# Kernel optimization log

Measured on AMD Instinct MI355X. Metric: run time of the kernel, lower is better.

The kernel has to match this reference:

```python
import jax, jax.numpy as jnp
import numpy as np
import math

B, L, D = 2, 2048, 1024
H = 16
DH = D // H  # 64
XPOS_SCALE_BASE = 512.0
THETA = 10000.0


def setup_inputs() -> dict:
    key = jax.random.key(0)
    ks = jax.random.split(key, 9)
    s = 0.02  # keep logits in a sane range like trained weights
    return {
        "x": jax.random.normal(ks[0], (B, L, D), dtype=jnp.float32),
        "Wq": jax.random.normal(ks[1], (D, D), dtype=jnp.float32) * s,
        "bq": jax.random.normal(ks[2], (D,), dtype=jnp.float32) * s,
        "Wk": jax.random.normal(ks[3], (D, D), dtype=jnp.float32) * s,
        "bk": jax.random.normal(ks[4], (D,), dtype=jnp.float32) * s,
        "Wv": jax.random.normal(ks[5], (D, D), dtype=jnp.float32) * s,
        "bv": jax.random.normal(ks[6], (D,), dtype=jnp.float32) * s,
        "Wo": jax.random.normal(ks[7], (D, D), dtype=jnp.float32) * s,
        "bo": jax.random.normal(ks[8], (D,), dtype=jnp.float32) * s,
    }


def _rotate_half(t):
    # pairwise interleaved rotation, as in rotary_embedding_torch
    t1 = t[..., 0::2]
    t2 = t[..., 1::2]
    return jnp.stack([-t2, t1], axis=-1).reshape(t.shape)


def _xpos_rotate(q, k):
    # q, k: [B, H, L, DH]; xPos rotary embedding (use_xpos=True)
    seq = q.shape[2]
    half = jnp.arange(0, DH, 2, dtype=jnp.float32)
    inv_freq = 1.0 / (THETA ** (half / DH))            # [DH/2]
    t = jnp.arange(seq, dtype=jnp.float32)             # [L]
    freqs = t[:, None] * inv_freq[None, :]             # [L, DH/2]
    freqs = jnp.repeat(freqs, 2, axis=-1)              # [L, DH] interleaved
    # xPos length-extrapolatable scale
    scale_vec = (half + 0.4 * DH) / (1.4 * DH)         # [DH/2]
    power = (t - seq // 2) / XPOS_SCALE_BASE           # [L]
    scale = scale_vec[None, :] ** power[:, None]       # [L, DH/2]
    scale = jnp.repeat(scale, 2, axis=-1)              # [L, DH]
    cos = jnp.cos(freqs)
    sin = jnp.sin(freqs)
    q_out = q * (cos * scale) + _rotate_half(q) * (sin * scale)
    k_out = k * (cos / scale) + _rotate_half(k) * (sin / scale)
    return q_out, k_out


def reference(x, Wq, bq, Wk, bk, Wv, bv, Wo, bo):
    b, l, d = x.shape
    # projections; note source swaps names: v_mat <- k-proj, k_mat <- v-proj
    q = (x @ Wq.T + bq).reshape(b, l, H, DH).transpose(0, 2, 1, 3)  # [b,h,l,dh]
    v = (x @ Wk.T + bk).reshape(b, l, H, DH).transpose(0, 2, 1, 3)
    k = (x @ Wv.T + bv).reshape(b, l, H, DH).transpose(0, 2, 1, 3)
    q, k = _xpos_rotate(q, k)
    # source divides by sqrt(Dh * num_heads) == sqrt(dim)
    scores = jnp.einsum("bhqd,bhkd->bhqk", q, k) / math.sqrt(d)
    weights = jax.nn.softmax(scores, axis=-1)
    inter = jnp.einsum("bhqk,bhkd->bhqd", weights, v)
    inter = inter.transpose(0, 2, 1, 3).reshape(b, l, d)
    return inter @ Wo.T + bo
```

## Files before the change

### kernel.cpp

```cpp
#include <hip/hip_runtime.h>
#include <math.h>

#define NB 2
#define NL 2048
#define ND 1024
#define NH 16
#define NDH 64
#define NBL 4096

typedef __attribute__((ext_vector_type(4)))  float f32x4;
typedef __attribute__((ext_vector_type(16))) float f32x16;
typedef __attribute__((ext_vector_type(8)))  short s16x8;
typedef __attribute__((ext_vector_type(4)))  short s16x4;

#define LOG2E 1.44269504088896f

__device__ __forceinline__ float fexp2(float x){
#if __has_builtin(__builtin_amdgcn_exp2f)
  return __builtin_amdgcn_exp2f(x);
#else
  return exp2f(x);
#endif
}

__device__ __forceinline__ unsigned short f2bf(float f){
  unsigned int u = __float_as_uint(f);
  u += 0x7FFF + ((u >> 16) & 1);
  return (unsigned short)(u >> 16);
}

__device__ __forceinline__ unsigned int pk2bf(float lo, float hi){
  return __builtin_amdgcn_perm(__float_as_uint(hi) + 0x8000u,
                               __float_as_uint(lo) + 0x8000u, 0x07060302u);
}

__global__ void cvt_all(const float* __restrict__ x,
                        const float* __restrict__ wq, const float* __restrict__ wk,
                        const float* __restrict__ wv, const float* __restrict__ wo,
                        unsigned short* __restrict__ xb,
                        unsigned short* __restrict__ wqb, unsigned short* __restrict__ wkb,
                        unsigned short* __restrict__ wvb, unsigned short* __restrict__ wob){
  int i = blockIdx.x * blockDim.x + threadIdx.x;
  const float* s; unsigned short* d; int off;
  if (i < (1<<20)) { s = x; d = xb; off = i; }
  else {
    int j = i - (1<<20); int w = j >> 18; off = j & ((1<<18)-1);
    s = (w==0)?wq:(w==1)?wk:(w==2)?wv:wo;
    d = (w==0)?wqb:(w==1)?wkb:(w==2)?wvb:wob;
  }
  float4 f = reinterpret_cast<const float4*>(s)[off];
  ushort4 r; r.x=f2bf(f.x); r.y=f2bf(f.y); r.z=f2bf(f.z); r.w=f2bf(f.w);
  reinterpret_cast<ushort4*>(d)[off] = r;
}

__global__ void rope_tables(float2* __restrict__ qtab, float2* __restrict__ ktab){
  int t = blockIdx.x * blockDim.x + threadIdx.x;
  int l = t >> 5, i = t & 31;
  float half = 2.0f * (float)i;
  float inv_freq = 1.0f / powf(10000.0f, half / 64.0f);
  float fr = (float)l * inv_freq;
  float sv = (half + 0.4f * 64.0f) / (1.4f * 64.0f);
  float pw = ((float)l - 1024.0f) / 512.0f;
  float sc = powf(sv, pw);
  float cs = cosf(fr), sn = sinf(fr);
  qtab[t] = make_float2(cs * sc, sn * sc);
  ktab[t] = make_float2(cs / sc, sn / sc);
}

__device__ __forceinline__ void gemm_core128(
    const unsigned short* __restrict__ A, const unsigned short* __restrict__ W,
    int row0, int col0,
    unsigned short (&As)[128][32], unsigned short (&Bs)[128][32],
    f32x4 (&acc)[4][4])
{
  const int tid  = threadIdx.x;
  const int wave = tid >> 6, lane = tid & 63;
  const int m16  = lane & 15, quad = lane >> 4;
  const int mrow = (wave & 1) * 64, ncol = (wave >> 1) * 64;
  const int rA   = lane >> 2, cA = (lane & 3) * 8;

  for (int k0 = 0; k0 < ND; k0 += 32){
    __syncthreads();
#pragma unroll
    for (int i2 = 0; i2 < 2; i2++){
      const int c = wave * 2 + i2;
      const unsigned short* ga = A + (size_t)(row0 + c*16 + rA) * ND + k0 + cA;
      const unsigned short* gb = W + (size_t)(col0 + c*16 + rA) * ND + k0 + cA;
      __builtin_amdgcn_global_load_lds((const __attribute__((address_space(1))) void*)ga,
                                       (__attribute__((address_space(3))) void*)&As[c*16][0], 16, 0, 0);
      __builtin_amdgcn_global_load_lds((const __attribute__((address_space(1))) void*)gb,
                                       (__attribute__((address_space(3))) void*)&Bs[c*16][0], 16, 0, 0);
    }
    __syncthreads();
    s16x8 af[4], bf[4];
#pragma unroll
    for (int mt = 0; mt < 4; mt++) af[mt] = *reinterpret_cast<const s16x8*>(&As[mrow + mt*16 + m16][quad*8]);
#pragma unroll
    for (int nt = 0; nt < 4; nt++) bf[nt] = *reinterpret_cast<const s16x8*>(&Bs[ncol + nt*16 + m16][quad*8]);
#pragma unroll
    for (int mt = 0; mt < 4; mt++)
#pragma unroll
      for (int nt = 0; nt < 4; nt++)
        acc[mt][nt] = __builtin_amdgcn_mfma_f32_16x16x32_bf16(af[mt], bf[nt], acc[mt][nt], 0, 0, 0);
  }
}

__global__ __launch_bounds__(256) void gemm_qkv(
    const unsigned short* __restrict__ A,
    const unsigned short* __restrict__ Wq, const float* __restrict__ bq,
    const unsigned short* __restrict__ Wk, const float* __restrict__ bk,
    const unsigned short* __restrict__ Wv, const float* __restrict__ bv,
    unsigned short* __restrict__ qb, unsigned short* __restrict__ kb,
    unsigned short* __restrict__ vtb,
    const float2* __restrict__ qtab, const float2* __restrict__ ktab)
{
  __shared__ unsigned short As[128][32];
  __shared__ unsigned short Bs[128][32];
  __shared__ unsigned short T[128][72];

  const int mode = blockIdx.z;
  const unsigned short* W = (mode==0) ? Wq : (mode==1) ? Wk : Wv;
  const float* bias       = (mode==0) ? bq : (mode==1) ? bk : bv;

  const int row0 = blockIdx.x * 128, col0 = blockIdx.y * 128;
  f32x4 acc[4][4] = {};
  gemm_core128(A, W, row0, col0, As, Bs, acc);

  const int tid  = threadIdx.x;
  const int wave = tid >> 6, lane = tid & 63;
  const int m16  = lane & 15, quad = lane >> 4;
  const int mrow = (wave & 1) * 64, ncol = (wave >> 1) * 64;

  if (mode == 2){
    const int b = row0 >> 11, l0 = row0 & (NL - 1);
#pragma unroll
    for (int h2 = 0; h2 < 2; h2++){
      __syncthreads();
      if ((wave >> 1) == h2){
#pragma unroll
        for (int mt = 0; mt < 4; mt++)
#pragma unroll
          for (int nt = 0; nt < 4; nt++)
#pragma unroll
            for (int r = 0; r < 4; r++){
              int lrow = mrow + mt*16 + quad*4 + r;
              int dh   = nt*16 + m16;
              T[lrow][dh] = f2bf(acc[mt][nt][r] + bias[col0 + h2*64 + dh]);
            }
      }
      __syncthreads();
      const int bh = b * NH + (col0 >> 6) + h2;
#pragma unroll
      for (int j4 = 0; j4 < 4; j4++){
        int c = tid * 4 + j4;
        int d = c >> 4, seg = (c & 15) * 8;
        unsigned short tmp[8];
#pragma unroll
        for (int jj = 0; jj < 8; jj++) tmp[jj] = T[seg + jj][d];
        *reinterpret_cast<uint4*>(vtb + (size_t)(bh * NDH + d) * NL + l0 + seg) =
            *reinterpret_cast<uint4*>(tmp);
      }
    }
  } else {
    const float qscale = (mode == 0) ? (0.03125f * LOG2E) : 1.0f;
    const float2* tab  = (mode == 0) ? qtab : ktab;
    unsigned short* dst = (mode == 0) ? qb : kb;
#pragma unroll
    for (int mt = 0; mt < 4; mt++)
#pragma unroll
      for (int nt = 0; nt < 4; nt++)
#pragma unroll
        for (int r = 0; r < 4; r++){
          int grow = row0 + mrow + mt*16 + quad*4 + r;
          int gcol = col0 + ncol + nt*16 + m16;
          float v = acc[mt][nt][r] + bias[gcol];
          int b = grow >> 11, l = grow & (NL - 1);
          int h = gcol >> 6, dh = gcol & 63;
          float pv = __shfl_xor(v, 1);
          float2 t = tab[l*32 + (dh >> 1)];
          float rh = (dh & 1) ? pv : -pv;
          float ov = (v * t.x + rh * t.y) * qscale;
          dst[(((size_t)(b * NH + h)) * NL + l) * NDH + dh] = f2bf(ov);
        }
  }
}

__global__ __launch_bounds__(256) void gemm_o(
    const unsigned short* __restrict__ A, const unsigned short* __restrict__ W,
    const float* __restrict__ bias, float* __restrict__ out)
{
  __shared__ unsigned short As[128][32];
  __shared__ unsigned short Bs[64][32];
  const int tid  = threadIdx.x;
  const int wave = tid >> 6, lane = tid & 63;
  const int m16  = lane & 15, quad = lane >> 4;
  const int mrow = (wave & 1) * 64, ncol = (wave >> 1) * 32;
  const int rA   = lane >> 2, cA = (lane & 3) * 8;
  const int row0 = blockIdx.x * 128, col0 = blockIdx.y * 64;

  f32x4 acc[4][2] = {};

  for (int k0 = 0; k0 < ND; k0 += 32){
    __syncthreads();
#pragma unroll
    for (int i3 = 0; i3 < 3; i3++){
      const int c = wave * 3 + i3;
      const unsigned short* g; unsigned short* l;
      if (c < 8){ g = A + (size_t)(row0 + c*16 + rA) * ND + k0 + cA;      l = &As[c*16][0]; }
      else      { g = W + (size_t)(col0 + (c-8)*16 + rA) * ND + k0 + cA;  l = &Bs[(c-8)*16][0]; }
      __builtin_amdgcn_global_load_lds((const __attribute__((address_space(1))) void*)g,
                                       (__attribute__((address_space(3))) void*)l, 16, 0, 0);
    }
    __syncthreads();
    s16x8 af[4], bf[2];
#pragma unroll
    for (int mt = 0; mt < 4; mt++) af[mt] = *reinterpret_cast<const s16x8*>(&As[mrow + mt*16 + m16][quad*8]);
#pragma unroll
    for (int nt = 0; nt < 2; nt++) bf[nt] = *reinterpret_cast<const s16x8*>(&Bs[ncol + nt*16 + m16][quad*8]);
#pragma unroll
    for (int mt = 0; mt < 4; mt++)
#pragma unroll
      for (int nt = 0; nt < 2; nt++)
        acc[mt][nt] = __builtin_amdgcn_mfma_f32_16x16x32_bf16(af[mt], bf[nt], acc[mt][nt], 0, 0, 0);
  }

#pragma unroll
  for (int mt = 0; mt < 4; mt++)
#pragma unroll
    for (int nt = 0; nt < 2; nt++)
#pragma unroll
      for (int r = 0; r < 4; r++){
        int grow = row0 + mrow + mt*16 + quad*4 + r;
        int gcol = col0 + ncol + nt*16 + m16;
        out[(size_t)grow * ND + gcol] = acc[mt][nt][r] + bias[gcol];
      }
}

__global__ __launch_bounds__(256, 1) void attn_kernel(
    const unsigned short* __restrict__ qb,
    const unsigned short* __restrict__ kb,
    const unsigned short* __restrict__ vtb,
    unsigned short* __restrict__ ob)
{
  __shared__ unsigned short smem[256 * 72];
  const int tid  = threadIdx.x;
  const int wave = tid >> 6, lane = tid & 63;
  const int l31  = lane & 31, g = lane >> 5;
  const int bh   = blockIdx.y;
  const int q0   = blockIdx.x * 256;
  const unsigned short* Q  = qb  + (size_t)bh * NL * NDH;
  const unsigned short* K  = kb  + (size_t)bh * NL * NDH;
  const unsigned short* Vt = vtb + (size_t)bh * NDH * NL;

  s16x8 qf[2][4];
#pragma unroll
  for (int q2 = 0; q2 < 2; q2++)
#pragma unroll
    for (int s = 0; s < 4; s++)
      qf[q2][s] = *reinterpret_cast<const s16x8*>(
          Q + (size_t)(q0 + wave*64 + q2*32 + l31) * NDH + s*16 + g*8);

  const int r0 = tid >> 3,          c0 = tid & 7;
  const int r1 = (tid + 256) >> 3,  c1 = tid & 7;
  const int so0 = r0*64 + ((c0 ^ (r0 & 7)) * 8);
  const int so1 = r1*64 + ((c1 ^ (r1 & 7)) * 8);

  uint4 kreg0 = *reinterpret_cast<const uint4*>(K  + (size_t)r0 * NDH + c0*8);
  uint4 kreg1 = *reinterpret_cast<const uint4*>(K  + (size_t)r1 * NDH + c1*8);
  uint4 vreg0 = *reinterpret_cast<const uint4*>(Vt + (size_t)r0 * NL  + c0*8);
  uint4 vreg1 = *reinterpret_cast<const uint4*>(Vt + (size_t)r1 * NL  + c1*8);
  *reinterpret_cast<uint4*>(&smem[so0])         = kreg0;
  *reinterpret_cast<uint4*>(&smem[so1])         = kreg1;
  *reinterpret_cast<uint4*>(&smem[8192 + so0])  = vreg0;
  *reinterpret_cast<uint4*>(&smem[8192 + so1])  = vreg1;
  kreg0 = *reinterpret_cast<const uint4*>(K  + (size_t)(64 + r0) * NDH + c0*8);
  kreg1 = *reinterpret_cast<const uint4*>(K  + (size_t)(64 + r1) * NDH + c1*8);
  vreg0 = *reinterpret_cast<const uint4*>(Vt + (size_t)r0 * NL + 64 + c0*8);
  vreg1 = *reinterpret_cast<const uint4*>(Vt + (size_t)r1 * NL + 64 + c1*8);
  __syncthreads();

  float ls[2] = {0.f, 0.f};
  f32x16 ot[2][2] = {};
  const int key7 = l31 & 7;

  for (int kt = 0; kt < 32; kt++){
    const int cur = (kt & 1) * 4096;
    const int nxt = 4096 - cur;
    if (kt < 31){
      *reinterpret_cast<uint4*>(&smem[nxt + so0])        = kreg0;
      *reinterpret_cast<uint4*>(&smem[nxt + so1])        = kreg1;
      *reinterpret_cast<uint4*>(&smem[8192 + nxt + so0]) = vreg0;
      *reinterpret_cast<uint4*>(&smem[8192 + nxt + so1]) = vreg1;
    }
    if (kt < 30){
      const int k0n = (kt + 2) * 64;
      kreg0 = *reinterpret_cast<const uint4*>(K  + (size_t)(k0n + r0) * NDH + c0*8);
      kreg1 = *reinterpret_cast<const uint4*>(K  + (size_t)(k0n + r1) * NDH + c1*8);
      vreg0 = *reinterpret_cast<const uint4*>(Vt + (size_t)r0 * NL + k0n + c0*8);
      vreg1 = *reinterpret_cast<const uint4*>(Vt + (size_t)r1 * NL + k0n + c1*8);
    }

    const unsigned short* Kb = &smem[cur];
    const unsigned short* Vb = &smem[8192 + cur];

    unsigned int pe[2][2][8];
#pragma unroll
    for (int t = 0; t < 2; t++){
      f32x16 st0 = {}, st1 = {};
#pragma unroll
      for (int s = 0; s < 4; s++){
        const int cg = (2*s + g) ^ key7;
        s16x8 kf = *reinterpret_cast<const s16x8*>(&Kb[(t*32 + l31)*64 + cg*8]);
        st0 = __builtin_amdgcn_mfma_f32_32x32x16_bf16(kf, qf[0][s], st0, 0, 0, 0);
        st1 = __builtin_amdgcn_mfma_f32_32x32x16_bf16(kf, qf[1][s], st1, 0, 0, 0);
      }
#pragma unroll
      for (int i = 0; i < 8; i++){
        float a0 = fexp2(st0[2*i]), a1 = fexp2(st0[2*i+1]);
        ls[0] += a0 + a1;
        pe[0][t][i] = pk2bf(a0, a1);
        float b0 = fexp2(st1[2*i]), b1 = fexp2(st1[2*i+1]);
        ls[1] += b0 + b1;
        pe[1][t][i] = pk2bf(b0, b1);
      }
    }

#pragma unroll
    for (int mt = 0; mt < 2; mt++){
      const int dh = mt*32 + l31;
#pragma unroll
      for (int s = 0; s < 8; s++){
        const int cg = s ^ (dh & 7);
        s16x4 vf = *reinterpret_cast<const s16x4*>(&Vb[dh*64 + cg*8 + g*4]);
        uint2 pb0; pb0.x = pe[0][s>>2][2*(s&3)]; pb0.y = pe[0][s>>2][2*(s&3)+1];
        ot[mt][0] = __builtin_amdgcn_mfma_f32_32x32x8bf16_1k(
            vf, *reinterpret_cast<s16x4*>(&pb0), ot[mt][0], 0, 0, 0);
        uint2 pb1; pb1.x = pe[1][s>>2][2*(s&3)]; pb1.y = pe[1][s>>2][2*(s&3)+1];
        ot[mt][1] = __builtin_amdgcn_mfma_f32_32x32x8bf16_1k(
            vf, *reinterpret_cast<s16x4*>(&pb1), ot[mt][1], 0, 0, 0);
      }
    }
    __syncthreads();
  }

  float linv[2];
#pragma unroll
  for (int q2 = 0; q2 < 2; q2++){
    float t = ls[q2] + __shfl_xor(ls[q2], 32);
    linv[q2] = 1.0f / t;
  }

#pragma unroll
  for (int mt = 0; mt < 2; mt++)
#pragma unroll
    for (int q2 = 0; q2 < 2; q2++)
#pragma unroll
      for (int s = 0; s < 4; s++){
        float o0 = ot[mt][q2][4*s    ] * linv[q2];
        float o1 = ot[mt][q2][4*s + 1] * linv[q2];
        float o2 = ot[mt][q2][4*s + 2] * linv[q2];
        float o3 = ot[mt][q2][4*s + 3] * linv[q2];
        uint2 pk; pk.x = pk2bf(o0, o1); pk.y = pk2bf(o2, o3);
        *reinterpret_cast<uint2*>(&smem[(wave*64 + q2*32 + l31)*72 + mt*32 + s*8 + g*4]) = pk;
      }
  __syncthreads();

  const int bb = bh >> 4, h = bh & 15;
#pragma unroll
  for (int j = 0; j < 8; j++){
    int idx = j*256 + tid;
    int row = idx >> 3, cg2 = (idx & 7) * 8;
    *reinterpret_cast<uint4*>(ob + ((size_t)(bb*NL + q0 + row)) * ND + h*NDH + cg2) =
        *reinterpret_cast<const uint4*>(&smem[row*72 + cg2]);
  }
}

extern "C" void kernel_launch(void* const* d_in, const int* in_sizes, int n_in,
                              void* d_out, int out_size, void* d_ws, size_t ws_size,
                              hipStream_t stream)
{
  (void)in_sizes; (void)n_in; (void)out_size; (void)ws_size;
  const float* x  = (const float*)d_in[0];
  const float* Wq = (const float*)d_in[1];
  const float* bq = (const float*)d_in[2];
  const float* Wk = (const float*)d_in[3];
  const float* bk = (const float*)d_in[4];
  const float* Wv = (const float*)d_in[5];
  const float* bv = (const float*)d_in[6];
  const float* Wo = (const float*)d_in[7];
  const float* bo = (const float*)d_in[8];
  float* out = (float*)d_out;

  char* p = (char*)d_ws;
  unsigned short* xb   = (unsigned short*)p; p += (size_t)NBL*ND*2;
  unsigned short* wqb  = (unsigned short*)p; p += (size_t)ND*ND*2;
  unsigned short* wkb  = (unsigned short*)p; p += (size_t)ND*ND*2;
  unsigned short* wvb  = (unsigned short*)p; p += (size_t)ND*ND*2;
  unsigned short* wob  = (unsigned short*)p; p += (size_t)ND*ND*2;
  unsigned short* qbuf = (unsigned short*)p; p += (size_t)NBL*ND*2;
  unsigned short* kbuf = (unsigned short*)p; p += (size_t)NBL*ND*2;
  unsigned short* vtb  = (unsigned short*)p; p += (size_t)NBL*ND*2;
  unsigned short* ibuf = (unsigned short*)p; p += (size_t)NBL*ND*2;
  float2* qtab = (float2*)p; p += (size_t)NL*32*8;
  float2* ktab = (float2*)p; p += (size_t)NL*32*8;

  hipLaunchKernelGGL(cvt_all, dim3(8192), dim3(256), 0, stream,
                     x, Wq, Wk, Wv, Wo, xb, wqb, wkb, wvb, wob);
  hipLaunchKernelGGL(rope_tables, dim3(NL*32/256), dim3(256), 0, stream, qtab, ktab);

  hipLaunchKernelGGL(gemm_qkv, dim3(NBL/128, ND/128, 3), dim3(256), 0, stream,
                     xb, wqb, bq, wvb, bv, wkb, bk, qbuf, kbuf, vtb, qtab, ktab);

  hipLaunchKernelGGL(attn_kernel, dim3(NL/256, NB*NH), dim3(256), 0, stream,
                     qbuf, kbuf, vtb, ibuf);

  hipLaunchKernelGGL(gemm_o, dim3(NBL/128, ND/64), dim3(256), 0, stream, ibuf, wob, bo, out);
}
```

Before: 208.9 us.

## Split attention over key halves and add a combine kernel

Splits each attention block's key range into two halves via a third grid dimension, doubling the number of blocks, and allows two blocks per CU. Each half writes unnormalized bf16 partial outputs and row sums; a new combine kernel adds the partials and normalizes before the output projection. This targets the low occupancy of one block per CU in the attention kernel. In exchange it adds an extra kernel pass over the partial buffers and an extra bf16 rounding of partials. The P-fragment packing is also reorganized into uint2 pairs.

```diff
diff --git a/kernel.cpp b/kernel.cpp
--- a/kernel.cpp
+++ b/kernel.cpp
@@ -236,18 +236,21 @@
       }
 }
 
-__global__ __launch_bounds__(256, 1) void attn_kernel(
+__global__ __launch_bounds__(256, 2) void attn_kernel(
     const unsigned short* __restrict__ qb,
     const unsigned short* __restrict__ kb,
     const unsigned short* __restrict__ vtb,
-    unsigned short* __restrict__ ob)
+    unsigned short* __restrict__ opart,
+    float* __restrict__ lsum)
 {
   __shared__ unsigned short smem[256 * 72];
   const int tid  = threadIdx.x;
   const int wave = tid >> 6, lane = tid & 63;
   const int l31  = lane & 31, g = lane >> 5;
   const int bh   = blockIdx.y;
+  const int z    = blockIdx.z;
   const int q0   = blockIdx.x * 256;
+  const int kbase = z * (NL / 2);
   const unsigned short* Q  = qb  + (size_t)bh * NL * NDH;
   const unsigned short* K  = kb  + (size_t)bh * NL * NDH;
   const unsigned short* Vt = vtb + (size_t)bh * NDH * NL;
@@ -260,50 +263,50 @@
       qf[q2][s] = *reinterpret_cast<const s16x8*>(
           Q + (size_t)(q0 + wave*64 + q2*32 + l31) * NDH + s*16 + g*8);
 
-  const int r0 = tid >> 3,          c0 = tid & 7;
-  const int r1 = (tid + 256) >> 3,  c1 = tid & 7;
+  const int r0 = tid >> 3, c0 = tid & 7;
+  const int r1 = r0 + 32;
   const int so0 = r0*64 + ((c0 ^ (r0 & 7)) * 8);
-  const int so1 = r1*64 + ((c1 ^ (r1 & 7)) * 8);
-
-  uint4 kreg0 = *reinterpret_cast<const uint4*>(K  + (size_t)r0 * NDH + c0*8);
-  uint4 kreg1 = *reinterpret_cast<const uint4*>(K  + (size_t)r1 * NDH + c1*8);
-  uint4 vreg0 = *reinterpret_cast<const uint4*>(Vt + (size_t)r0 * NL  + c0*8);
-  uint4 vreg1 = *reinterpret_cast<const uint4*>(Vt + (size_t)r1 * NL  + c1*8);
+  const int so1 = r1*64 + ((c0 ^ (r1 & 7)) * 8);
+
+  uint4 kreg0 = *reinterpret_cast<const uint4*>(K  + (size_t)(kbase + r0) * NDH + c0*8);
+  uint4 kreg1 = *reinterpret_cast<const uint4*>(K  + (size_t)(kbase + r1) * NDH + c0*8);
+  uint4 vreg0 = *reinterpret_cast<const uint4*>(Vt + (size_t)r0 * NL + kbase + c0*8);
+  uint4 vreg1 = *reinterpret_cast<const uint4*>(Vt + (size_t)r1 * NL + kbase + c0*8);
   *reinterpret_cast<uint4*>(&smem[so0])         = kreg0;
   *reinterpret_cast<uint4*>(&smem[so1])         = kreg1;
   *reinterpret_cast<uint4*>(&smem[8192 + so0])  = vreg0;
   *reinterpret_cast<uint4*>(&smem[8192 + so1])  = vreg1;
-  kreg0 = *reinterpret_cast<const uint4*>(K  + (size_t)(64 + r0) * NDH + c0*8);
-  kreg1 = *reinterpret_cast<const uint4*>(K  + (size_t)(64 + r1) * NDH + c1*8);
-  vreg0 = *reinterpret_cast<const uint4*>(Vt + (size_t)r0 * NL + 64 + c0*8);
-  vreg1 = *reinterpret_cast<const uint4*>(Vt + (size_t)r1 * NL + 64 + c1*8);
+  kreg0 = *reinterpret_cast<const uint4*>(K  + (size_t)(kbase + 64 + r0) * NDH + c0*8);
+  kreg1 = *reinterpret_cast<const uint4*>(K  + (size_t)(kbase + 64 + r1) * NDH + c0*8);
+  vreg0 = *reinterpret_cast<const uint4*>(Vt + (size_t)r0 * NL + kbase + 64 + c0*8);
+  vreg1 = *reinterpret_cast<const uint4*>(Vt + (size_t)r1 * NL + kbase + 64 + c0*8);
   __syncthreads();
 
   float ls[2] = {0.f, 0.f};
   f32x16 ot[2][2] = {};
   const int key7 = l31 & 7;
 
-  for (int kt = 0; kt < 32; kt++){
+  for (int kt = 0; kt < 16; kt++){
     const int cur = (kt & 1) * 4096;
     const int nxt = 4096 - cur;
-    if (kt < 31){
+    if (kt < 15){
       *reinterpret_cast<uint4*>(&smem[nxt + so0])        = kreg0;
       *reinterpret_cast<uint4*>(&smem[nxt + so1])        = kreg1;
       *reinterpret_cast<uint4*>(&smem[8192 + nxt + so0]) = vreg0;
       *reinterpret_cast<uint4*>(&smem[8192 + nxt + so1]) = vreg1;
     }
-    if (kt < 30){
-      const int k0n = (kt + 2) * 64;
+    if (kt < 14){
+      const int k0n = kbase + (kt + 2) * 64;
       kreg0 = *reinterpret_cast<const uint4*>(K  + (size_t)(k0n + r0) * NDH + c0*8);
-      kreg1 = *reinterpret_cast<const uint4*>(K  + (size_t)(k0n + r1) * NDH + c1*8);
+      kreg1 = *reinterpret_cast<const uint4*>(K  + (size_t)(k0n + r1) * NDH + c0*8);
       vreg0 = *reinterpret_cast<const uint4*>(Vt + (size_t)r0 * NL + k0n + c0*8);
-      vreg1 = *reinterpret_cast<const uint4*>(Vt + (size_t)r1 * NL + k0n + c1*8);
+      vreg1 = *reinterpret_cast<const uint4*>(Vt + (size_t)r1 * NL + k0n + c0*8);
     }
 
     const unsigned short* Kb = &smem[cur];
     const unsigned short* Vb = &smem[8192 + cur];
 
-    unsigned int pe[2][2][8];
+    uint2 pmat[2][8];
 #pragma unroll
     for (int t = 0; t < 2; t++){
       f32x16 st0 = {}, st1 = {};
@@ -315,13 +318,17 @@
         st1 = __builtin_amdgcn_mfma_f32_32x32x16_bf16(kf, qf[1][s], st1, 0, 0, 0);
       }
 #pragma unroll
-      for (int i = 0; i < 8; i++){
-        float a0 = fexp2(st0[2*i]), a1 = fexp2(st0[2*i+1]);
-        ls[0] += a0 + a1;
-        pe[0][t][i] = pk2bf(a0, a1);
-        float b0 = fexp2(st1[2*i]), b1 = fexp2(st1[2*i+1]);
-        ls[1] += b0 + b1;
-        pe[1][t][i] = pk2bf(b0, b1);
+      for (int j = 0; j < 4; j++){
+        float a0 = fexp2(st0[4*j]), a1 = fexp2(st0[4*j+1]);
+        float a2 = fexp2(st0[4*j+2]), a3 = fexp2(st0[4*j+3]);
+        ls[0] += (a0 + a1) + (a2 + a3);
+        pmat[0][t*4+j].x = pk2bf(a0, a1);
+        pmat[0][t*4+j].y = pk2bf(a2, a3);
+        float b0 = fexp2(st1[4*j]), b1 = fexp2(st1[4*j+1]);
+        float b2 = fexp2(st1[4*j+2]), b3 = fexp2(st1[4*j+3]);
+        ls[1] += (b0 + b1) + (b2 + b3);
+        pmat[1][t*4+j].x = pk2bf(b0, b1);
+        pmat[1][t*4+j].y = pk2bf(b2, b3);
       }
     }
 
@@ -332,22 +339,20 @@
       for (int s = 0; s < 8; s++){
         const int cg = s ^ (dh & 7);
         s16x4 vf = *reinterpret_cast<const s16x4*>(&Vb[dh*64 + cg*8 + g*4]);
-        uint2 pb0; pb0.x = pe[0][s>>2][2*(s&3)]; pb0.y = pe[0][s>>2][2*(s&3)+1];
         ot[mt][0] = __builtin_amdgcn_mfma_f32_32x32x8bf16_1k(
-            vf, *reinterpret_cast<s16x4*>(&pb0), ot[mt][0], 0, 0, 0);
-        uint2 pb1; pb1.x = pe[1][s>>2][2*(s&3)]; pb1.y = pe[1][s>>2][2*(s&3)+1];
+            vf, *reinterpret_cast<s16x4*>(&pmat[0][s]), ot[mt][0], 0, 0, 0);
         ot[mt][1] = __builtin_amdgcn_mfma_f32_32x32x8bf16_1k(
-            vf, *reinterpret_cast<s16x4*>(&pb1), ot[mt][1], 0, 0, 0);
+            vf, *reinterpret_cast<s16x4*>(&pmat[1][s]), ot[mt][1], 0, 0, 0);
       }
     }
     __syncthreads();
   }
 
-  float linv[2];
 #pragma unroll
   for (int q2 = 0; q2 < 2; q2++){
     float t = ls[q2] + __shfl_xor(ls[q2], 32);
-    linv[q2] = 1.0f / t;
+    if (g == 0)
+      lsum[((size_t)z * NB * NH + bh) * NL + q0 + wave*64 + q2*32 + l31] = t;
   }
 
 #pragma unroll
@@ -356,23 +361,50 @@
     for (int q2 = 0; q2 < 2; q2++)
 #pragma unroll
       for (int s = 0; s < 4; s++){
-        float o0 = ot[mt][q2][4*s    ] * linv[q2];
-        float o1 = ot[mt][q2][4*s + 1] * linv[q2];
-        float o2 = ot[mt][q2][4*s + 2] * linv[q2];
-        float o3 = ot[mt][q2][4*s + 3] * linv[q2];
-        uint2 pk; pk.x = pk2bf(o0, o1); pk.y = pk2bf(o2, o3);
+        uint2 pk;
+        pk.x = pk2bf(ot[mt][q2][4*s], ot[mt][q2][4*s + 1]);
+        pk.y = pk2bf(ot[mt][q2][4*s + 2], ot[mt][q2][4*s + 3]);
         *reinterpret_cast<uint2*>(&smem[(wave*64 + q2*32 + l31)*72 + mt*32 + s*8 + g*4]) = pk;
       }
   __syncthreads();
 
   const int bb = bh >> 4, h = bh & 15;
+  unsigned short* od = opart + (size_t)z * NBL * ND;
 #pragma unroll
   for (int j = 0; j < 8; j++){
     int idx = j*256 + tid;
     int row = idx >> 3, cg2 = (idx & 7) * 8;
-    *reinterpret_cast<uint4*>(ob + ((size_t)(bb*NL + q0 + row)) * ND + h*NDH + cg2) =
+    *reinterpret_cast<uint4*>(od + ((size_t)(bb*NL + q0 + row)) * ND + h*NDH + cg2) =
         *reinterpret_cast<const uint4*>(&smem[row*72 + cg2]);
   }
+}
+
+__device__ __forceinline__ unsigned int comb2(unsigned int a, unsigned int b, float inv){
+  float alo = __uint_as_float(a << 16), ahi = __uint_as_float(a & 0xFFFF0000u);
+  float blo = __uint_as_float(b << 16), bhi = __uint_as_float(b & 0xFFFF0000u);
+  return pk2bf((alo + blo) * inv, (ahi + bhi) * inv);
+}
+
+__global__ __launch_bounds__(256) void attn_combine(
+    unsigned short* __restrict__ opart, const float* __restrict__ lsum)
+{
+  int idx = blockIdx.x * 256 + threadIdx.x;
+  int row = idx >> 7;
+  int col8 = idx & 127;
+  int h = col8 >> 3;
+  int b = row >> 11, l = row & (NL - 1);
+  int bh = b * NH + h;
+  float l0 = lsum[(size_t)bh * NL + l];
+  float l1 = lsum[(size_t)(NB*NH + bh) * NL + l];
+  float inv = 1.0f / (l0 + l1);
+  uint4 u0 = reinterpret_cast<const uint4*>(opart)[idx];
+  uint4 u1 = reinterpret_cast<const uint4*>(opart + (size_t)NBL * ND)[idx];
+  uint4 o;
+  o.x = comb2(u0.x, u1.x, inv);
+  o.y = comb2(u0.y, u1.y, inv);
+  o.z = comb2(u0.z, u1.z, inv);
+  o.w = comb2(u0.w, u1.w, inv);
+  reinterpret_cast<uint4*>(opart)[idx] = o;
 }
 
 extern "C" void kernel_launch(void* const* d_in, const int* in_sizes, int n_in,
@@ -392,15 +424,16 @@
   float* out = (float*)d_out;
 
   char* p = (char*)d_ws;
-  unsigned short* xb   = (unsigned short*)p; p += (size_t)NBL*ND*2;
-  unsigned short* wqb  = (unsigned short*)p; p += (size_t)ND*ND*2;
-  unsigned short* wkb  = (unsigned short*)p; p += (size_t)ND*ND*2;
-  unsigned short* wvb  = (unsigned short*)p; p += (size_t)ND*ND*2;
-  unsigned short* wob  = (unsigned short*)p; p += (size_t)ND*ND*2;
-  unsigned short* qbuf = (unsigned short*)p; p += (size_t)NBL*ND*2;
-  unsigned short* kbuf = (unsigned short*)p; p += (size_t)NBL*ND*2;
-  unsigned short* vtb  = (unsigned short*)p; p += (size_t)NBL*ND*2;
-  unsigned short* ibuf = (unsigned short*)p; p += (size_t)NBL*ND*2;
+  unsigned short* xb    = (unsigned short*)p; p += (size_t)NBL*ND*2;
+  unsigned short* wqb   = (unsigned short*)p; p += (size_t)ND*ND*2;
+  unsigned short* wkb   = (unsigned short*)p; p += (size_t)ND*ND*2;
+  unsigned short* wvb   = (unsigned short*)p; p += (size_t)ND*ND*2;
+  unsigned short* wob   = (unsigned short*)p; p += (size_t)ND*ND*2;
+  unsigned short* qbuf  = (unsigned short*)p; p += (size_t)NBL*ND*2;
+  unsigned short* kbuf  = (unsigned short*)p; p += (size_t)NBL*ND*2;
+  unsigned short* vtb   = (unsigned short*)p; p += (size_t)NBL*ND*2;
+  unsigned short* opart = (unsigned short*)p; p += (size_t)2*NBL*ND*2;
+  float* lsum = (float*)p; p += (size_t)2*NB*NH*NL*4;
   float2* qtab = (float2*)p; p += (size_t)NL*32*8;
   float2* ktab = (float2*)p; p += (size_t)NL*32*8;
 
@@ -411,8 +444,9 @@
   hipLaunchKernelGGL(gemm_qkv, dim3(NBL/128, ND/128, 3), dim3(256), 0, stream,
                      xb, wqb, bq, wvb, bv, wkb, bk, qbuf, kbuf, vtb, qtab, ktab);
 
-  hipLaunchKernelGGL(attn_kernel, dim3(NL/256, NB*NH), dim3(256), 0, stream,
-                     qbuf, kbuf, vtb, ibuf);
-
-  hipLaunchKernelGGL(gemm_o, dim3(NBL/128, ND/64), dim3(256), 0, stream, ibuf, wob, bo, out);
-}
+  hipLaunchKernelGGL(attn_kernel, dim3(NL/256, NB*NH, 2), dim3(256), 0, stream,
+                     qbuf, kbuf, vtb, opart, lsum);
+  hipLaunchKernelGGL(attn_combine, dim3(NBL*ND/8/256), dim3(256), 0, stream, opart, lsum);
+
+  hipLaunchKernelGGL(gemm_o, dim3(NBL/128, ND/64), dim3(256), 0, stream, opart, wob, bo, out);
+}
```

Result: no change. 207.7 us (-0.6%).
